# Kernel tuning notes

Hardware: AMD Instinct MI355X
Metric: run time of the kernel (lower is better)

The kernel has to match this reference:

```python
import jax, jax.numpy as jnp
import numpy as np

HIDDEN = 512
DETER = 1024
STOCH = 32
OBS = 1024
ACT = 64
B, T = 64, 256


def _linear_params(key, out_dim, in_dim):
    kw, kb = jax.random.split(key)
    scale = 1.0 / np.sqrt(in_dim)
    W = jax.random.uniform(kw, (out_dim, in_dim), jnp.float32, -scale, scale)
    b = jax.random.uniform(kb, (out_dim,), jnp.float32, -scale, scale)
    return W, b


def setup_inputs() -> dict:
    key = jax.random.key(0)
    ks = jax.random.split(key, 12)
    obs_embeds = jax.random.normal(ks[0], (B, T, OBS), jnp.float32)
    action_embs = jax.random.normal(ks[1], (B, T, ACT), jnp.float32)
    noise_prior = jax.random.normal(ks[2], (B, T, STOCH), jnp.float32)
    noise_post = jax.random.normal(ks[3], (B, T, STOCH), jnp.float32)
    W_sa, b_sa = _linear_params(ks[4], DETER, STOCH + ACT)
    W_ih, b_ih = _linear_params(ks[5], 3 * DETER, DETER)
    W_hh, b_hh = _linear_params(ks[6], 3 * DETER, DETER)
    Wp1, bp1 = _linear_params(ks[7], HIDDEN, DETER)
    Wp2, bp2 = _linear_params(ks[8], 2 * STOCH, HIDDEN)
    Wq1, bq1 = _linear_params(ks[9], HIDDEN, DETER + OBS)
    Wq2, bq2 = _linear_params(ks[10], 2 * STOCH, HIDDEN)
    return {
        "obs_embeds": obs_embeds, "action_embs": action_embs,
        "noise_prior": noise_prior, "noise_post": noise_post,
        "W_sa": W_sa, "b_sa": b_sa,
        "W_ih": W_ih, "b_ih": b_ih, "W_hh": W_hh, "b_hh": b_hh,
        "Wp1": Wp1, "bp1": bp1, "Wp2": Wp2, "bp2": bp2,
        "Wq1": Wq1, "bq1": bq1, "Wq2": Wq2, "bq2": bq2,
    }


def _rollout(obs_embeds, action_embs, noise_prior, noise_post,
             W_sa, b_sa, W_ih, b_ih, W_hh, b_hh,
             Wp1, bp1, Wp2, bp2, Wq1, bq1, Wq2, bq2):
    S = Wp2.shape[0] // 2
    eps = 1e-5

    def gru(x, h):  # torch GRUCell: gates ordered r, z, n
        gi = x @ W_ih.T + b_ih
        gh = h @ W_hh.T + b_hh
        ir, iz, inn = jnp.split(gi, 3, axis=-1)
        hr, hz, hn = jnp.split(gh, 3, axis=-1)
        r = jax.nn.sigmoid(ir + hr)
        z = jax.nn.sigmoid(iz + hz)
        n = jnp.tanh(inn + r * hn)
        return (1.0 - z) * n + z * h

    def step(carry, inp):
        deter, stoch = carry
        obs, act, n_p, n_q = inp
        # prior: h_t = f(s_{t-1}, a_{t-1}, h_{t-1})
        emb = jax.nn.relu(jnp.concatenate([stoch, act], -1) @ W_sa.T + b_sa)
        deter = gru(emb, deter)
        pm_s = jax.nn.relu(deter @ Wp1.T + bp1) @ Wp2.T + bp2
        p_mean = pm_s[..., :S]
        p_std = jax.nn.softplus(pm_s[..., S:]) + eps
        p_stoch = p_mean + p_std * n_p
        # posterior: p(s_t | h_t, o_t)
        qm_s = jax.nn.relu(jnp.concatenate([deter, obs], -1) @ Wq1.T + bq1) @ Wq2.T + bq2
        q_mean = qm_s[..., :S]
        q_std = jax.nn.softplus(qm_s[..., S:]) + eps
        q_stoch = q_mean + q_std * n_q
        out = jnp.concatenate([deter, p_mean, p_std, p_stoch, q_mean, q_std, q_stoch], -1)
        return (deter, q_stoch), out

    batch = obs_embeds.shape[0]
    deter0 = jnp.zeros((batch, W_hh.shape[1]), obs_embeds.dtype)
    stoch0 = jnp.zeros((batch, S), obs_embeds.dtype)
    xs = (
        jnp.swapaxes(obs_embeds, 0, 1),
        jnp.swapaxes(action_embs, 0, 1),
        jnp.swapaxes(noise_prior, 0, 1),
        jnp.swapaxes(noise_post, 0, 1),
    )
    _, outs = jax.lax.scan(step, (deter0, stoch0), xs)
    return jnp.swapaxes(outs, 0, 1)  # [B, T, deter + 6*stoch]


def reference(obs_embeds, action_embs, noise_prior, noise_post,
              W_sa, b_sa, W_ih, b_ih, W_hh, b_hh,
              Wp1, bp1, Wp2, bp2, Wq1, bq1, Wq2, bq2):
    return _rollout(obs_embeds, action_embs, noise_prior, noise_post,
                    W_sa, b_sa, W_ih, b_ih, W_hh, b_hh,
                    Wp1, bp1, Wp2, bp2, Wq1, bq1, Wq2, bq2)
```

## Files before the change

kernel.cpp:

```cpp
#include <hip/hip_runtime.h>
#include <math.h>

#define B_   64
#define T_   256
#define OUTD 1216

typedef unsigned short ushort_t;
typedef unsigned int   uint32;
typedef __attribute__((ext_vector_type(8))) short bfrag;
typedef __attribute__((ext_vector_type(4))) float f32x4;
typedef __attribute__((ext_vector_type(4))) unsigned short us4;

__device__ __forceinline__ float sigmoidf_(float x) { return 1.0f / (1.0f + __expf(-x)); }
__device__ __forceinline__ float softplusf_(float x) { return (x > 20.0f) ? x : log1pf(__expf(x)); }
__device__ __forceinline__ ushort_t f2bf(float f) {
    uint32 u = __float_as_uint(f);
    u += 0x7fffu + ((u >> 16) & 1u);
    return (ushort_t)(u >> 16);
}
__device__ __forceinline__ float bf2f(ushort_t u) { return __uint_as_float(((uint32)u) << 16); }

__global__ void kwprep(const float* __restrict__ Wih, const float* __restrict__ Whh,
                       const float* __restrict__ Wp1, const float* __restrict__ Wq1,
                       const float* __restrict__ Wp2, const float* __restrict__ Wq2,
                       const float* __restrict__ Wsa,
                       ushort_t* Wih_b, ushort_t* Whh_b, ushort_t* Wp1_b, ushort_t* Wq1_b,
                       ushort_t* W2sw, ushort_t* Wsasw) {
    int stride = gridDim.x * blockDim.x;
    int gid = blockIdx.x * blockDim.x + threadIdx.x;
    for (int i = gid; i < 3072 * 1024; i += stride) Wih_b[i] = f2bf(Wih[i]);
    for (int i = gid; i < 3072 * 1024; i += stride) Whh_b[i] = f2bf(Whh[i]);
    for (int i = gid; i < 512 * 1024; i += stride) Wp1_b[i] = f2bf(Wp1[i]);
    for (int i = gid; i < 512 * 2048; i += stride) Wq1_b[i] = f2bf(Wq1[i]);
    for (int i = gid; i < 65536; i += stride) {
        int head = i >> 15, g = (i >> 9) & 63, o = (i >> 3) & 63, ii = i & 7;
        const float* src = head ? Wq2 : Wp2;
        W2sw[i] = f2bf(src[o * 512 + g * 8 + ii]);
    }
    for (int i = gid; i < 98304; i += stride) {
        int g = i >> 13, j = (i >> 3) & 1023, ii = i & 7;
        Wsasw[i] = f2bf(Wsa[j * 96 + g * 8 + ii]);
    }
}

__global__ void kinit(const float* __restrict__ act, const float* __restrict__ Wsa,
                      const float* __restrict__ bsa,
                      ushort_t* emb_sw, ushort_t* det_sw0, float* det_fp0) {
    int gid = blockIdx.x * 256 + threadIdx.x;
    int j = gid >> 6, b = gid & 63;
    float acc = bsa[j];
    const float* a = act + (size_t)b * T_ * 64;
    const float* w = Wsa + j * 96 + 32;
#pragma unroll 8
    for (int c = 0; c < 64; ++c) acc += a[c] * w[c];
    emb_sw[((j >> 3) * 64 + b) * 8 + (j & 7)] = f2bf(fmaxf(acc, 0.f));
    det_sw0[gid] = 0;
    det_fp0[gid] = 0.f;
}

__global__ __launch_bounds__(256) void kgru(int t,
        const ushort_t* __restrict__ Wih, const ushort_t* __restrict__ Whh,
        const float* __restrict__ bih, const float* __restrict__ bhh,
        const ushort_t* __restrict__ emb_sw, const ushort_t* __restrict__ det_sw_in,
        const float* __restrict__ det_fp_in,
        ushort_t* __restrict__ det_sw_out, float* __restrict__ det_fp_out,
        const float* __restrict__ obs, ushort_t* __restrict__ obs_sw,
        float* __restrict__ out) {
    if (blockIdx.x >= 64) {
        int kb = (blockIdx.x - 64) * 64;
        int tx = threadIdx.x & 63, ty = threadIdx.x >> 6;
        for (int b = ty; b < 64; b += 4) {
            int k = kb + tx;
            float v = obs[((size_t)b * T_ + t) * 1024 + k];
            obs_sw[((k >> 3) * 64 + b) * 8 + (k & 7)] = f2bf(v);
        }
        return;
    }
    __shared__ float red[2 * 24 * 256];
    const int tid = threadIdx.x;
    const int lane = tid & 63, w = tid >> 6;
    const int m = lane & 15, quad = lane >> 4;
    const int j0 = blockIdx.x * 16;

    f32x4 acc[2][3][4];
#pragma unroll
    for (int a2 = 0; a2 < 2; ++a2)
#pragma unroll
        for (int g = 0; g < 3; ++g)
#pragma unroll
            for (int n = 0; n < 4; ++n) acc[a2][g][n] = (f32x4){0.f, 0.f, 0.f, 0.f};

    const int kb0 = w * 256;
    const ushort_t* arow[2][3];
#pragma unroll
    for (int g = 0; g < 3; ++g) {
        arow[0][g] = Wih + (size_t)(g * 1024 + j0 + m) * 1024 + kb0 + quad * 8;
        arow[1][g] = Whh + (size_t)(g * 1024 + j0 + m) * 1024 + kb0 + quad * 8;
    }
    const ushort_t* bx = emb_sw + ((kb0 >> 3) + quad) * 512 + m * 8;
    const ushort_t* bh = det_sw_in + ((kb0 >> 3) + quad) * 512 + m * 8;

#pragma unroll
    for (int it = 0; it < 8; ++it) {
        bfrag a[2][3], vx[4], vh[4];
#pragma unroll
        for (int g = 0; g < 3; ++g) {
            a[0][g] = *(const bfrag*)(arow[0][g] + it * 32);
            a[1][g] = *(const bfrag*)(arow[1][g] + it * 32);
        }
#pragma unroll
        for (int n = 0; n < 4; ++n) {
            vx[n] = *(const bfrag*)(bx + it * 2048 + n * 128);
            vh[n] = *(const bfrag*)(bh + it * 2048 + n * 128);
        }
#pragma unroll
        for (int g = 0; g < 3; ++g)
#pragma unroll
            for (int n = 0; n < 4; ++n) {
                acc[0][g][n] = __builtin_amdgcn_mfma_f32_16x16x32_bf16(a[0][g], vx[n], acc[0][g][n], 0, 0, 0);
                acc[1][g][n] = __builtin_amdgcn_mfma_f32_16x16x32_bf16(a[1][g], vh[n], acc[1][g][n], 0, 0, 0);
            }
    }

    if (w & 1) {
        float* dst = red + (w >> 1) * 6144;
#pragma unroll
        for (int a2 = 0; a2 < 2; ++a2)
#pragma unroll
            for (int g = 0; g < 3; ++g)
#pragma unroll
                for (int n = 0; n < 4; ++n)
                    *(f32x4*)(dst + ((a2 * 3 + g) * 4 + n) * 256 + lane * 4) = acc[a2][g][n];
    }
    __syncthreads();
    if (!(w & 1)) {
        float* dst = red + (w >> 1) * 6144;
#pragma unroll
        for (int a2 = 0; a2 < 2; ++a2)
#pragma unroll
            for (int g = 0; g < 3; ++g)
#pragma unroll
                for (int n = 0; n < 4; ++n) {
                    float* pp = dst + ((a2 * 3 + g) * 4 + n) * 256 + lane * 4;
                    f32x4 v = *(const f32x4*)pp;
                    v += acc[a2][g][n];
                    *(f32x4*)pp = v;
                }
    }
    __syncthreads();

    int b = tid >> 2, jq = tid & 3;
    int nt = b >> 4, bl = b & 15;
    int lsrc = (jq * 16 + bl) * 4;
    float gg[2][3][4];
#pragma unroll
    for (int a2 = 0; a2 < 2; ++a2)
#pragma unroll
        for (int g = 0; g < 3; ++g) {
            f32x4 v0 = *(const f32x4*)(red + ((a2 * 3 + g) * 4 + nt) * 256 + lsrc);
            f32x4 v1 = *(const f32x4*)(red + 6144 + ((a2 * 3 + g) * 4 + nt) * 256 + lsrc);
#pragma unroll
            for (int i = 0; i < 4; ++i) gg[a2][g][i] = v0[i] + v1[i];
        }
    f32x4 bi[3], bh2[3];
#pragma unroll
    for (int g = 0; g < 3; ++g) {
        bi[g] = *(const f32x4*)(bih + g * 1024 + j0 + jq * 4);
        bh2[g] = *(const f32x4*)(bhh + g * 1024 + j0 + jq * 4);
    }
    f32x4 h4;
    us4 dq;
#pragma unroll
    for (int i = 0; i < 4; ++i) {
        int j = j0 + jq * 4 + i;
        float r = sigmoidf_(gg[0][0][i] + bi[0][i] + gg[1][0][i] + bh2[0][i]);
        float z = sigmoidf_(gg[0][1][i] + bi[1][i] + gg[1][1][i] + bh2[1][i]);
        float n = tanhf(gg[0][2][i] + bi[2][i] + r * (gg[1][2][i] + bh2[2][i]));
        float hp = det_fp_in[j * 64 + b];
        float h = (1.f - z) * n + z * hp;
        h4[i] = h;
        dq[i] = f2bf(h);
        det_fp_out[j * 64 + b] = h;
    }
    *(f32x4*)(out + ((size_t)b * T_ + t) * OUTD + j0 + jq * 4) = h4;
    int kbase = j0 + jq * 4;
    *(us4*)(det_sw_out + ((kbase >> 3) * 64 + b) * 8 + (kbase & 7)) = dq;
}

__global__ __launch_bounds__(256) void khid(
        const ushort_t* __restrict__ Wp1b, const float* __restrict__ bp1,
        const ushort_t* __restrict__ Wq1b, const float* __restrict__ bq1,
        const ushort_t* __restrict__ det_sw, const ushort_t* __restrict__ obs_sw,
        float* __restrict__ pm1, float* __restrict__ qm1) {
    __shared__ float red[4 * 4 * 256];
    const int tid = threadIdx.x;
    const int lane = tid & 63, w = tid >> 6;
    const int m = lane & 15, quad = lane >> 4;
    const bool isq = blockIdx.x >= 32;
    const int j0 = (isq ? blockIdx.x - 32 : blockIdx.x) * 16;

    f32x4 acc[4];
#pragma unroll
    for (int n = 0; n < 4; ++n) acc[n] = (f32x4){0.f, 0.f, 0.f, 0.f};

    if (!isq) {
        const ushort_t* ar = Wp1b + (size_t)(j0 + m) * 1024 + w * 256 + quad * 8;
        const ushort_t* bb = det_sw + ((w * 32) + quad) * 512 + m * 8;
#pragma unroll
        for (int it = 0; it < 8; ++it) {
            bfrag a = *(const bfrag*)(ar + it * 32);
#pragma unroll
            for (int n = 0; n < 4; ++n) {
                bfrag v = *(const bfrag*)(bb + it * 2048 + n * 128);
                acc[n] = __builtin_amdgcn_mfma_f32_16x16x32_bf16(a, v, acc[n], 0, 0, 0);
            }
        }
    } else {
        int kb0 = w * 512;
        const ushort_t* bsrc = (w < 2) ? det_sw : obs_sw;
        int kloc = (w < 2) ? kb0 : kb0 - 1024;
        const ushort_t* ar = Wq1b + (size_t)(j0 + m) * 2048 + kb0 + quad * 8;
        const ushort_t* bb = bsrc + ((kloc >> 3) + quad) * 512 + m * 8;
#pragma unroll
        for (int it = 0; it < 16; ++it) {
            bfrag a = *(const bfrag*)(ar + it * 32);
#pragma unroll
            for (int n = 0; n < 4; ++n) {
                bfrag v = *(const bfrag*)(bb + it * 2048 + n * 128);
                acc[n] = __builtin_amdgcn_mfma_f32_16x16x32_bf16(a, v, acc[n], 0, 0, 0);
            }
        }
    }
#pragma unroll
    for (int n = 0; n < 4; ++n)
        *(f32x4*)(red + (w * 4 + n) * 256 + lane * 4) = acc[n];
    __syncthreads();

    int b = tid >> 2, jq = tid & 3;
    int nt = b >> 4, lsrc = (jq * 16 + (b & 15)) * 4;
    f32x4 s = (f32x4){0.f, 0.f, 0.f, 0.f};
#pragma unroll
    for (int w2 = 0; w2 < 4; ++w2) s += *(const f32x4*)(red + (w2 * 4 + nt) * 256 + lsrc);
    f32x4 bv = *(const f32x4*)((isq ? bq1 : bp1) + j0 + jq * 4);
    f32x4 r;
#pragma unroll
    for (int i = 0; i < 4; ++i) r[i] = fmaxf(s[i] + bv[i], 0.f);
    *(f32x4*)((isq ? qm1 : pm1) + (size_t)b * 512 + j0 + jq * 4) = r;
}

__global__ __launch_bounds__(256) void khead(int t,
        const float* __restrict__ pm1, const float* __restrict__ qm1,
        const float* __restrict__ bp2, const float* __restrict__ bq2,
        const ushort_t* __restrict__ W2sw, const ushort_t* __restrict__ Wsasw,
        const float* __restrict__ bsa,
        const float* __restrict__ n_p, const float* __restrict__ n_q,
        const float* __restrict__ act,
        float* __restrict__ out, ushort_t* __restrict__ emb_sw) {
    __shared__ float sh[1024 + 128 + 96];
    float* s_p = sh;
    float* s_q = sh + 512;
    float* s_head = sh + 1024;
    float* s_in = sh + 1152;
    const int b = blockIdx.x, tid = threadIdx.x;
    if (tid < 128) ((f32x4*)s_p)[tid] = ((const f32x4*)(pm1 + (size_t)b * 512))[tid];
    else ((f32x4*)s_q)[tid - 128] = ((const f32x4*)(qm1 + (size_t)b * 512))[tid - 128];
    if (t + 1 < T_ && tid < 64) s_in[32 + tid] = act[((size_t)b * T_ + t + 1) * 64 + tid];
    __syncthreads();
    if (tid < 128) {
        int head = tid >> 6, o = tid & 63;
        const ushort_t* wp = W2sw + head * 32768 + o * 8;
        const float* hv = head ? s_q : s_p;
        float acc2 = (head ? bq2 : bp2)[o];
#pragma unroll 4
        for (int g = 0; g < 64; ++g) {
            bfrag w8 = *(const bfrag*)(wp + g * 512);
#pragma unroll
            for (int i2 = 0; i2 < 8; ++i2) acc2 += hv[g * 8 + i2] * bf2f((ushort_t)w8[i2]);
        }
        s_head[tid] = acc2;
    }
    __syncthreads();
    if (tid < 64) {
        int s = tid & 31, isq = tid >> 5;
        float mean = s_head[isq * 64 + s];
        float raw = s_head[isq * 64 + 32 + s];
        float sd = softplusf_(raw) + 1e-5f;
        float noise = (isq ? n_q : n_p)[((size_t)b * T_ + t) * 32 + s];
        float st = mean + sd * noise;
        float* o = out + ((size_t)b * T_ + t) * OUTD + 1024 + isq * 96;
        o[s] = mean;
        o[32 + s] = sd;
        o[64 + s] = st;
        if (isq) s_in[s] = st;
    }
    __syncthreads();
    if (t + 1 < T_) {
#pragma unroll
        for (int q = 0; q < 4; ++q) {
            int j = q * 256 + tid;
            float acc2 = bsa[j];
#pragma unroll
            for (int g = 0; g < 12; ++g) {
                bfrag w8 = *(const bfrag*)(Wsasw + ((size_t)g * 1024 + j) * 8);
#pragma unroll
                for (int i2 = 0; i2 < 8; ++i2) acc2 += s_in[g * 8 + i2] * bf2f((ushort_t)w8[i2]);
            }
            emb_sw[((j >> 3) * 64 + b) * 8 + (j & 7)] = f2bf(fmaxf(acc2, 0.f));
        }
    }
}

extern "C" void kernel_launch(void* const* d_in, const int* in_sizes, int n_in,
                              void* d_out, int out_size, void* d_ws, size_t ws_size,
                              hipStream_t stream) {
    const float* obs = (const float*)d_in[0];
    const float* act = (const float*)d_in[1];
    const float* n_p = (const float*)d_in[2];
    const float* n_q = (const float*)d_in[3];
    const float* W_sa = (const float*)d_in[4];
    const float* b_sa = (const float*)d_in[5];
    const float* W_ih = (const float*)d_in[6];
    const float* b_ih = (const float*)d_in[7];
    const float* W_hh = (const float*)d_in[8];
    const float* b_hh = (const float*)d_in[9];
    const float* Wp1 = (const float*)d_in[10];
    const float* bp1 = (const float*)d_in[11];
    const float* Wp2 = (const float*)d_in[12];
    const float* bp2 = (const float*)d_in[13];
    const float* Wq1 = (const float*)d_in[14];
    const float* bq1 = (const float*)d_in[15];
    const float* Wq2 = (const float*)d_in[16];
    const float* bq2 = (const float*)d_in[17];
    float* out = (float*)d_out;

    char* p = (char*)d_ws;
    ushort_t* Wih_b = (ushort_t*)p;  p += (size_t)3145728 * 2;
    ushort_t* Whh_b = (ushort_t*)p;  p += (size_t)3145728 * 2;
    ushort_t* Wp1_b = (ushort_t*)p;  p += (size_t)524288 * 2;
    ushort_t* Wq1_b = (ushort_t*)p;  p += (size_t)1048576 * 2;
    ushort_t* W2sw  = (ushort_t*)p;  p += (size_t)65536 * 2;
    ushort_t* Wsasw = (ushort_t*)p;  p += (size_t)98304 * 2;
    ushort_t* emb_sw = (ushort_t*)p; p += (size_t)65536 * 2;
    ushort_t* obs_sw = (ushort_t*)p; p += (size_t)65536 * 2;
    ushort_t* det_sw0 = (ushort_t*)p; p += (size_t)65536 * 2;
    ushort_t* det_sw1 = (ushort_t*)p; p += (size_t)65536 * 2;
    float* det_fp0 = (float*)p; p += (size_t)65536 * 4;
    float* det_fp1 = (float*)p; p += (size_t)65536 * 4;
    float* pm1 = (float*)p; p += (size_t)32768 * 4;
    float* qm1 = (float*)p; p += (size_t)32768 * 4;

    kwprep<<<1024, 256, 0, stream>>>(W_ih, W_hh, Wp1, Wq1, Wp2, Wq2, W_sa,
                                     Wih_b, Whh_b, Wp1_b, Wq1_b, W2sw, Wsasw);
    kinit<<<256, 256, 0, stream>>>(act, W_sa, b_sa, emb_sw, det_sw0, det_fp0);

    for (int t = 0; t < T_; ++t) {
        ushort_t* dsw_in = (t & 1) ? det_sw1 : det_sw0;
        ushort_t* dsw_out = (t & 1) ? det_sw0 : det_sw1;
        float* dfp_in = (t & 1) ? det_fp1 : det_fp0;
        float* dfp_out = (t & 1) ? det_fp0 : det_fp1;
        kgru<<<80, 256, 0, stream>>>(t, Wih_b, Whh_b, b_ih, b_hh, emb_sw, dsw_in, dfp_in,
                                     dsw_out, dfp_out, obs, obs_sw, out);
        khid<<<64, 256, 0, stream>>>(Wp1_b, bp1, Wq1_b, bq1, dsw_out, obs_sw, pm1, qm1);
        khead<<<64, 256, 0, stream>>>(t, pm1, qm1, bp2, bq2, W2sw, Wsasw, b_sa,
                                      n_p, n_q, act, out, emb_sw);
    }
}
```

Baseline: 10.24 ms.

## Fuse per-step kernels into one persistent rollout kernel with grid barriers

Replaces the 768 per-timestep launches (GRU, hidden, head kernels) with a single persistent kernel of 64 blocks that loops over all time steps. Stages are separated by a software grid barrier built on global atomics. Obs conversion moves into the head stage for the next step. This removes kernel launch overhead and launch gaps. The risks are that the barrier needs all 64 blocks co-resident, that spin-wait barriers carry their own latency, and that the obs conversion now uses only 64 blocks.

```diff
diff --git a/kernel.cpp b/kernel.cpp
--- a/kernel.cpp
+++ b/kernel.cpp
@@ -20,14 +20,32 @@
 }
 __device__ __forceinline__ float bf2f(ushort_t u) { return __uint_as_float(((uint32)u) << 16); }
 
+__device__ __forceinline__ void gbar(uint32* barf, int gen) {
+    __syncthreads();
+    if (threadIdx.x == 0) {
+        __threadfence();
+        uint32 old = __hip_atomic_fetch_add(barf + (gen & 1) * 32, 1u,
+                                            __ATOMIC_ACQ_REL, __HIP_MEMORY_SCOPE_AGENT);
+        if (old == 63u) {
+            __hip_atomic_store(barf + (gen & 1) * 32, 0u, __ATOMIC_RELAXED, __HIP_MEMORY_SCOPE_AGENT);
+            __hip_atomic_store(barf + 64, (uint32)gen, __ATOMIC_RELEASE, __HIP_MEMORY_SCOPE_AGENT);
+        }
+        while ((int)__hip_atomic_load(barf + 64, __ATOMIC_ACQUIRE, __HIP_MEMORY_SCOPE_AGENT) < gen)
+            __builtin_amdgcn_s_sleep(1);
+    }
+    __syncthreads();
+    __threadfence();
+}
+
 __global__ void kwprep(const float* __restrict__ Wih, const float* __restrict__ Whh,
                        const float* __restrict__ Wp1, const float* __restrict__ Wq1,
                        const float* __restrict__ Wp2, const float* __restrict__ Wq2,
                        const float* __restrict__ Wsa,
                        ushort_t* Wih_b, ushort_t* Whh_b, ushort_t* Wp1_b, ushort_t* Wq1_b,
-                       ushort_t* W2sw, ushort_t* Wsasw) {
+                       ushort_t* W2sw, ushort_t* Wsasw, uint32* barf) {
     int stride = gridDim.x * blockDim.x;
     int gid = blockIdx.x * blockDim.x + threadIdx.x;
+    if (gid < 256) barf[gid] = 0u;
     for (int i = gid; i < 3072 * 1024; i += stride) Wih_b[i] = f2bf(Wih[i]);
     for (int i = gid; i < 3072 * 1024; i += stride) Whh_b[i] = f2bf(Whh[i]);
     for (int i = gid; i < 512 * 1024; i += stride) Wp1_b[i] = f2bf(Wp1[i]);
@@ -43,270 +61,268 @@
     }
 }
 
-__global__ void kinit(const float* __restrict__ act, const float* __restrict__ Wsa,
-                      const float* __restrict__ bsa,
-                      ushort_t* emb_sw, ushort_t* det_sw0, float* det_fp0) {
-    int gid = blockIdx.x * 256 + threadIdx.x;
-    int j = gid >> 6, b = gid & 63;
-    float acc = bsa[j];
-    const float* a = act + (size_t)b * T_ * 64;
-    const float* w = Wsa + j * 96 + 32;
-#pragma unroll 8
-    for (int c = 0; c < 64; ++c) acc += a[c] * w[c];
-    emb_sw[((j >> 3) * 64 + b) * 8 + (j & 7)] = f2bf(fmaxf(acc, 0.f));
-    det_sw0[gid] = 0;
-    det_fp0[gid] = 0.f;
-}
-
-__global__ __launch_bounds__(256) void kgru(int t,
-        const ushort_t* __restrict__ Wih, const ushort_t* __restrict__ Whh,
-        const float* __restrict__ bih, const float* __restrict__ bhh,
-        const ushort_t* __restrict__ emb_sw, const ushort_t* __restrict__ det_sw_in,
-        const float* __restrict__ det_fp_in,
-        ushort_t* __restrict__ det_sw_out, float* __restrict__ det_fp_out,
-        const float* __restrict__ obs, ushort_t* __restrict__ obs_sw,
-        float* __restrict__ out) {
-    if (blockIdx.x >= 64) {
-        int kb = (blockIdx.x - 64) * 64;
-        int tx = threadIdx.x & 63, ty = threadIdx.x >> 6;
-        for (int b = ty; b < 64; b += 4) {
-            int k = kb + tx;
-            float v = obs[((size_t)b * T_ + t) * 1024 + k];
-            obs_sw[((k >> 3) * 64 + b) * 8 + (k & 7)] = f2bf(v);
-        }
-        return;
-    }
-    __shared__ float red[2 * 24 * 256];
-    const int tid = threadIdx.x;
+__global__ __launch_bounds__(256, 1) void krollout(
+        const ushort_t* Wih, const ushort_t* Whh,
+        const float* bih, const float* bhh,
+        const ushort_t* Wp1b, const float* bp1,
+        const ushort_t* Wq1b, const float* bq1,
+        const ushort_t* W2sw, const float* bp2, const float* bq2,
+        const ushort_t* Wsasw, const float* Wsa, const float* bsa,
+        const float* obs, const float* act,
+        const float* n_p, const float* n_q,
+        ushort_t* emb_sw, ushort_t* obs_sw,
+        ushort_t* det_sw0, ushort_t* det_sw1,
+        float* det_fp0, float* det_fp1,
+        float* pm1, float* qm1,
+        float* out, uint32* barf) {
+    __shared__ float red[12288];
+    const int bid = blockIdx.x, tid = threadIdx.x;
     const int lane = tid & 63, w = tid >> 6;
     const int m = lane & 15, quad = lane >> 4;
-    const int j0 = blockIdx.x * 16;
-
-    f32x4 acc[2][3][4];
-#pragma unroll
-    for (int a2 = 0; a2 < 2; ++a2)
-#pragma unroll
-        for (int g = 0; g < 3; ++g)
-#pragma unroll
-            for (int n = 0; n < 4; ++n) acc[a2][g][n] = (f32x4){0.f, 0.f, 0.f, 0.f};
-
-    const int kb0 = w * 256;
-    const ushort_t* arow[2][3];
-#pragma unroll
-    for (int g = 0; g < 3; ++g) {
-        arow[0][g] = Wih + (size_t)(g * 1024 + j0 + m) * 1024 + kb0 + quad * 8;
-        arow[1][g] = Whh + (size_t)(g * 1024 + j0 + m) * 1024 + kb0 + quad * 8;
-    }
-    const ushort_t* bx = emb_sw + ((kb0 >> 3) + quad) * 512 + m * 8;
-    const ushort_t* bh = det_sw_in + ((kb0 >> 3) + quad) * 512 + m * 8;
-
-#pragma unroll
-    for (int it = 0; it < 8; ++it) {
-        bfrag a[2][3], vx[4], vh[4];
-#pragma unroll
-        for (int g = 0; g < 3; ++g) {
-            a[0][g] = *(const bfrag*)(arow[0][g] + it * 32);
-            a[1][g] = *(const bfrag*)(arow[1][g] + it * 32);
-        }
-#pragma unroll
-        for (int n = 0; n < 4; ++n) {
-            vx[n] = *(const bfrag*)(bx + it * 2048 + n * 128);
-            vh[n] = *(const bfrag*)(bh + it * 2048 + n * 128);
-        }
-#pragma unroll
-        for (int g = 0; g < 3; ++g)
-#pragma unroll
-            for (int n = 0; n < 4; ++n) {
-                acc[0][g][n] = __builtin_amdgcn_mfma_f32_16x16x32_bf16(a[0][g], vx[n], acc[0][g][n], 0, 0, 0);
-                acc[1][g][n] = __builtin_amdgcn_mfma_f32_16x16x32_bf16(a[1][g], vh[n], acc[1][g][n], 0, 0, 0);
-            }
-    }
-
-    if (w & 1) {
-        float* dst = red + (w >> 1) * 6144;
-#pragma unroll
-        for (int a2 = 0; a2 < 2; ++a2)
-#pragma unroll
-            for (int g = 0; g < 3; ++g)
-#pragma unroll
-                for (int n = 0; n < 4; ++n)
-                    *(f32x4*)(dst + ((a2 * 3 + g) * 4 + n) * 256 + lane * 4) = acc[a2][g][n];
-    }
-    __syncthreads();
-    if (!(w & 1)) {
-        float* dst = red + (w >> 1) * 6144;
-#pragma unroll
-        for (int a2 = 0; a2 < 2; ++a2)
-#pragma unroll
-            for (int g = 0; g < 3; ++g)
+
+    *(f32x4*)(det_fp0 + bid * 1024 + tid * 4) = (f32x4){0.f, 0.f, 0.f, 0.f};
+    *(us4*)(det_sw0 + bid * 1024 + tid * 4) = (us4){0, 0, 0, 0};
+    {
+        int j0i = bid * 16;
+        for (int c4 = 0; c4 < 4; ++c4) {
+            int idx = c4 * 256 + tid;
+            int j = j0i + (idx >> 6), b2 = idx & 63;
+            float acc = bsa[j];
+            const float* a = act + (size_t)b2 * T_ * 64;
+            const float* ww = Wsa + j * 96 + 32;
+            for (int c = 0; c < 64; ++c) acc += a[c] * ww[c];
+            emb_sw[((j >> 3) * 64 + b2) * 8 + (j & 7)] = f2bf(fmaxf(acc, 0.f));
+        }
+        float4 v = *(const float4*)(obs + (size_t)bid * T_ * 1024 + tid * 4);
+        us4 o4; o4[0] = f2bf(v.x); o4[1] = f2bf(v.y); o4[2] = f2bf(v.z); o4[3] = f2bf(v.w);
+        int k = tid * 4;
+        *(us4*)(obs_sw + ((k >> 3) * 64 + bid) * 8 + (k & 7)) = o4;
+    }
+    int gen = 1;
+    gbar(barf, gen); ++gen;
+
+    for (int t = 0; t < T_; ++t) {
+        ushort_t* dsw_in  = (t & 1) ? det_sw1 : det_sw0;
+        ushort_t* dsw_out = (t & 1) ? det_sw0 : det_sw1;
+        float* dfp_in  = (t & 1) ? det_fp1 : det_fp0;
+        float* dfp_out = (t & 1) ? det_fp0 : det_fp1;
+
+        {
+            const int j0 = bid * 16;
+            f32x4 acc[2][3][4];
+#pragma unroll
+            for (int a2 = 0; a2 < 2; ++a2)
+#pragma unroll
+                for (int g = 0; g < 3; ++g)
+#pragma unroll
+                    for (int n = 0; n < 4; ++n) acc[a2][g][n] = (f32x4){0.f, 0.f, 0.f, 0.f};
+
+            const int kb0 = w * 256;
+            const ushort_t* arow[2][3];
+#pragma unroll
+            for (int g = 0; g < 3; ++g) {
+                arow[0][g] = Wih + (size_t)(g * 1024 + j0 + m) * 1024 + kb0 + quad * 8;
+                arow[1][g] = Whh + (size_t)(g * 1024 + j0 + m) * 1024 + kb0 + quad * 8;
+            }
+            const ushort_t* bx = emb_sw + ((kb0 >> 3) + quad) * 512 + m * 8;
+            const ushort_t* bh = dsw_in + ((kb0 >> 3) + quad) * 512 + m * 8;
+
+#pragma unroll
+            for (int it = 0; it < 8; ++it) {
+                bfrag a[2][3], vx[4], vh[4];
+#pragma unroll
+                for (int g = 0; g < 3; ++g) {
+                    a[0][g] = *(const bfrag*)(arow[0][g] + it * 32);
+                    a[1][g] = *(const bfrag*)(arow[1][g] + it * 32);
+                }
 #pragma unroll
                 for (int n = 0; n < 4; ++n) {
-                    float* pp = dst + ((a2 * 3 + g) * 4 + n) * 256 + lane * 4;
-                    f32x4 v = *(const f32x4*)pp;
-                    v += acc[a2][g][n];
-                    *(f32x4*)pp = v;
-                }
-    }
-    __syncthreads();
-
-    int b = tid >> 2, jq = tid & 3;
-    int nt = b >> 4, bl = b & 15;
-    int lsrc = (jq * 16 + bl) * 4;
-    float gg[2][3][4];
-#pragma unroll
-    for (int a2 = 0; a2 < 2; ++a2)
-#pragma unroll
-        for (int g = 0; g < 3; ++g) {
-            f32x4 v0 = *(const f32x4*)(red + ((a2 * 3 + g) * 4 + nt) * 256 + lsrc);
-            f32x4 v1 = *(const f32x4*)(red + 6144 + ((a2 * 3 + g) * 4 + nt) * 256 + lsrc);
-#pragma unroll
-            for (int i = 0; i < 4; ++i) gg[a2][g][i] = v0[i] + v1[i];
-        }
-    f32x4 bi[3], bh2[3];
-#pragma unroll
-    for (int g = 0; g < 3; ++g) {
-        bi[g] = *(const f32x4*)(bih + g * 1024 + j0 + jq * 4);
-        bh2[g] = *(const f32x4*)(bhh + g * 1024 + j0 + jq * 4);
-    }
-    f32x4 h4;
-    us4 dq;
-#pragma unroll
-    for (int i = 0; i < 4; ++i) {
-        int j = j0 + jq * 4 + i;
-        float r = sigmoidf_(gg[0][0][i] + bi[0][i] + gg[1][0][i] + bh2[0][i]);
-        float z = sigmoidf_(gg[0][1][i] + bi[1][i] + gg[1][1][i] + bh2[1][i]);
-        float n = tanhf(gg[0][2][i] + bi[2][i] + r * (gg[1][2][i] + bh2[2][i]));
-        float hp = det_fp_in[j * 64 + b];
-        float h = (1.f - z) * n + z * hp;
-        h4[i] = h;
-        dq[i] = f2bf(h);
-        det_fp_out[j * 64 + b] = h;
-    }
-    *(f32x4*)(out + ((size_t)b * T_ + t) * OUTD + j0 + jq * 4) = h4;
-    int kbase = j0 + jq * 4;
-    *(us4*)(det_sw_out + ((kbase >> 3) * 64 + b) * 8 + (kbase & 7)) = dq;
-}
-
-__global__ __launch_bounds__(256) void khid(
-        const ushort_t* __restrict__ Wp1b, const float* __restrict__ bp1,
-        const ushort_t* __restrict__ Wq1b, const float* __restrict__ bq1,
-        const ushort_t* __restrict__ det_sw, const ushort_t* __restrict__ obs_sw,
-        float* __restrict__ pm1, float* __restrict__ qm1) {
-    __shared__ float red[4 * 4 * 256];
-    const int tid = threadIdx.x;
-    const int lane = tid & 63, w = tid >> 6;
-    const int m = lane & 15, quad = lane >> 4;
-    const bool isq = blockIdx.x >= 32;
-    const int j0 = (isq ? blockIdx.x - 32 : blockIdx.x) * 16;
-
-    f32x4 acc[4];
-#pragma unroll
-    for (int n = 0; n < 4; ++n) acc[n] = (f32x4){0.f, 0.f, 0.f, 0.f};
-
-    if (!isq) {
-        const ushort_t* ar = Wp1b + (size_t)(j0 + m) * 1024 + w * 256 + quad * 8;
-        const ushort_t* bb = det_sw + ((w * 32) + quad) * 512 + m * 8;
-#pragma unroll
-        for (int it = 0; it < 8; ++it) {
-            bfrag a = *(const bfrag*)(ar + it * 32);
-#pragma unroll
-            for (int n = 0; n < 4; ++n) {
-                bfrag v = *(const bfrag*)(bb + it * 2048 + n * 128);
-                acc[n] = __builtin_amdgcn_mfma_f32_16x16x32_bf16(a, v, acc[n], 0, 0, 0);
-            }
-        }
-    } else {
-        int kb0 = w * 512;
-        const ushort_t* bsrc = (w < 2) ? det_sw : obs_sw;
-        int kloc = (w < 2) ? kb0 : kb0 - 1024;
-        const ushort_t* ar = Wq1b + (size_t)(j0 + m) * 2048 + kb0 + quad * 8;
-        const ushort_t* bb = bsrc + ((kloc >> 3) + quad) * 512 + m * 8;
-#pragma unroll
-        for (int it = 0; it < 16; ++it) {
-            bfrag a = *(const bfrag*)(ar + it * 32);
-#pragma unroll
-            for (int n = 0; n < 4; ++n) {
-                bfrag v = *(const bfrag*)(bb + it * 2048 + n * 128);
-                acc[n] = __builtin_amdgcn_mfma_f32_16x16x32_bf16(a, v, acc[n], 0, 0, 0);
-            }
-        }
-    }
-#pragma unroll
-    for (int n = 0; n < 4; ++n)
-        *(f32x4*)(red + (w * 4 + n) * 256 + lane * 4) = acc[n];
-    __syncthreads();
-
-    int b = tid >> 2, jq = tid & 3;
-    int nt = b >> 4, lsrc = (jq * 16 + (b & 15)) * 4;
-    f32x4 s = (f32x4){0.f, 0.f, 0.f, 0.f};
-#pragma unroll
-    for (int w2 = 0; w2 < 4; ++w2) s += *(const f32x4*)(red + (w2 * 4 + nt) * 256 + lsrc);
-    f32x4 bv = *(const f32x4*)((isq ? bq1 : bp1) + j0 + jq * 4);
-    f32x4 r;
-#pragma unroll
-    for (int i = 0; i < 4; ++i) r[i] = fmaxf(s[i] + bv[i], 0.f);
-    *(f32x4*)((isq ? qm1 : pm1) + (size_t)b * 512 + j0 + jq * 4) = r;
-}
-
-__global__ __launch_bounds__(256) void khead(int t,
-        const float* __restrict__ pm1, const float* __restrict__ qm1,
-        const float* __restrict__ bp2, const float* __restrict__ bq2,
-        const ushort_t* __restrict__ W2sw, const ushort_t* __restrict__ Wsasw,
-        const float* __restrict__ bsa,
-        const float* __restrict__ n_p, const float* __restrict__ n_q,
-        const float* __restrict__ act,
-        float* __restrict__ out, ushort_t* __restrict__ emb_sw) {
-    __shared__ float sh[1024 + 128 + 96];
-    float* s_p = sh;
-    float* s_q = sh + 512;
-    float* s_head = sh + 1024;
-    float* s_in = sh + 1152;
-    const int b = blockIdx.x, tid = threadIdx.x;
-    if (tid < 128) ((f32x4*)s_p)[tid] = ((const f32x4*)(pm1 + (size_t)b * 512))[tid];
-    else ((f32x4*)s_q)[tid - 128] = ((const f32x4*)(qm1 + (size_t)b * 512))[tid - 128];
-    if (t + 1 < T_ && tid < 64) s_in[32 + tid] = act[((size_t)b * T_ + t + 1) * 64 + tid];
-    __syncthreads();
-    if (tid < 128) {
-        int head = tid >> 6, o = tid & 63;
-        const ushort_t* wp = W2sw + head * 32768 + o * 8;
-        const float* hv = head ? s_q : s_p;
-        float acc2 = (head ? bq2 : bp2)[o];
+                    vx[n] = *(const bfrag*)(bx + it * 2048 + n * 128);
+                    vh[n] = *(const bfrag*)(bh + it * 2048 + n * 128);
+                }
+#pragma unroll
+                for (int g = 0; g < 3; ++g)
+#pragma unroll
+                    for (int n = 0; n < 4; ++n) {
+                        acc[0][g][n] = __builtin_amdgcn_mfma_f32_16x16x32_bf16(a[0][g], vx[n], acc[0][g][n], 0, 0, 0);
+                        acc[1][g][n] = __builtin_amdgcn_mfma_f32_16x16x32_bf16(a[1][g], vh[n], acc[1][g][n], 0, 0, 0);
+                    }
+            }
+            if (w & 1) {
+                float* dst = red + (w >> 1) * 6144;
+#pragma unroll
+                for (int a2 = 0; a2 < 2; ++a2)
+#pragma unroll
+                    for (int g = 0; g < 3; ++g)
+#pragma unroll
+                        for (int n = 0; n < 4; ++n)
+                            *(f32x4*)(dst + ((a2 * 3 + g) * 4 + n) * 256 + lane * 4) = acc[a2][g][n];
+            }
+            __syncthreads();
+            if (!(w & 1)) {
+                float* dst = red + (w >> 1) * 6144;
+#pragma unroll
+                for (int a2 = 0; a2 < 2; ++a2)
+#pragma unroll
+                    for (int g = 0; g < 3; ++g)
+#pragma unroll
+                        for (int n = 0; n < 4; ++n) {
+                            float* pp = dst + ((a2 * 3 + g) * 4 + n) * 256 + lane * 4;
+                            f32x4 v = *(const f32x4*)pp;
+                            v += acc[a2][g][n];
+                            *(f32x4*)pp = v;
+                        }
+            }
+            __syncthreads();
+            int b = tid >> 2, jq = tid & 3;
+            int nt = b >> 4, bl = b & 15;
+            int lsrc = (jq * 16 + bl) * 4;
+            float gg[2][3][4];
+#pragma unroll
+            for (int a2 = 0; a2 < 2; ++a2)
+#pragma unroll
+                for (int g = 0; g < 3; ++g) {
+                    f32x4 v0 = *(const f32x4*)(red + ((a2 * 3 + g) * 4 + nt) * 256 + lsrc);
+                    f32x4 v1 = *(const f32x4*)(red + 6144 + ((a2 * 3 + g) * 4 + nt) * 256 + lsrc);
+#pragma unroll
+                    for (int i = 0; i < 4; ++i) gg[a2][g][i] = v0[i] + v1[i];
+                }
+            f32x4 bi[3], bh2[3];
+#pragma unroll
+            for (int g = 0; g < 3; ++g) {
+                bi[g] = *(const f32x4*)(bih + g * 1024 + j0 + jq * 4);
+                bh2[g] = *(const f32x4*)(bhh + g * 1024 + j0 + jq * 4);
+            }
+            f32x4 h4;
+            us4 dq;
+#pragma unroll
+            for (int i = 0; i < 4; ++i) {
+                int j = j0 + jq * 4 + i;
+                float r = sigmoidf_(gg[0][0][i] + bi[0][i] + gg[1][0][i] + bh2[0][i]);
+                float z = sigmoidf_(gg[0][1][i] + bi[1][i] + gg[1][1][i] + bh2[1][i]);
+                float n = tanhf(gg[0][2][i] + bi[2][i] + r * (gg[1][2][i] + bh2[2][i]));
+                float hp = dfp_in[j * 64 + b];
+                float h = (1.f - z) * n + z * hp;
+                h4[i] = h;
+                dq[i] = f2bf(h);
+                dfp_out[j * 64 + b] = h;
+            }
+            *(f32x4*)(out + ((size_t)b * T_ + t) * OUTD + j0 + jq * 4) = h4;
+            int kbase = j0 + jq * 4;
+            *(us4*)(dsw_out + ((kbase >> 3) * 64 + b) * 8 + (kbase & 7)) = dq;
+        }
+        gbar(barf, gen); ++gen;
+
+        {
+            const bool isq = bid >= 32;
+            const int j0 = (isq ? bid - 32 : bid) * 16;
+            f32x4 acc[4];
+#pragma unroll
+            for (int n = 0; n < 4; ++n) acc[n] = (f32x4){0.f, 0.f, 0.f, 0.f};
+
+            if (!isq) {
+                const ushort_t* ar = Wp1b + (size_t)(j0 + m) * 1024 + w * 256 + quad * 8;
+                const ushort_t* bb = dsw_out + ((w * 32) + quad) * 512 + m * 8;
+#pragma unroll
+                for (int it = 0; it < 8; ++it) {
+                    bfrag a = *(const bfrag*)(ar + it * 32);
+#pragma unroll
+                    for (int n = 0; n < 4; ++n) {
+                        bfrag v = *(const bfrag*)(bb + it * 2048 + n * 128);
+                        acc[n] = __builtin_amdgcn_mfma_f32_16x16x32_bf16(a, v, acc[n], 0, 0, 0);
+                    }
+                }
+            } else {
+                int kb0 = w * 512;
+                const ushort_t* bsrc = (w < 2) ? dsw_out : obs_sw;
+                int kloc = (w < 2) ? kb0 : kb0 - 1024;
+                const ushort_t* ar = Wq1b + (size_t)(j0 + m) * 2048 + kb0 + quad * 8;
+                const ushort_t* bb = bsrc + ((kloc >> 3) + quad) * 512 + m * 8;
+#pragma unroll
+                for (int it = 0; it < 16; ++it) {
+                    bfrag a = *(const bfrag*)(ar + it * 32);
+#pragma unroll
+                    for (int n = 0; n < 4; ++n) {
+                        bfrag v = *(const bfrag*)(bb + it * 2048 + n * 128);
+                        acc[n] = __builtin_amdgcn_mfma_f32_16x16x32_bf16(a, v, acc[n], 0, 0, 0);
+                    }
+                }
+            }
+#pragma unroll
+            for (int n = 0; n < 4; ++n)
+                *(f32x4*)(red + (w * 4 + n) * 256 + lane * 4) = acc[n];
+            __syncthreads();
+            int b = tid >> 2, jq = tid & 3;
+            int nt = b >> 4, lsrc = (jq * 16 + (b & 15)) * 4;
+            f32x4 s = (f32x4){0.f, 0.f, 0.f, 0.f};
+#pragma unroll
+            for (int w2 = 0; w2 < 4; ++w2) s += *(const f32x4*)(red + (w2 * 4 + nt) * 256 + lsrc);
+            f32x4 bv = *(const f32x4*)((isq ? bq1 : bp1) + j0 + jq * 4);
+            f32x4 r;
+#pragma unroll
+            for (int i = 0; i < 4; ++i) r[i] = fmaxf(s[i] + bv[i], 0.f);
+            *(f32x4*)((isq ? qm1 : pm1) + (size_t)b * 512 + j0 + jq * 4) = r;
+        }
+        gbar(barf, gen); ++gen;
+
+        {
+            float* s_p = red;
+            float* s_q = red + 512;
+            float* s_head = red + 1024;
+            float* s_in = red + 1152;
+            const int bb = bid;
+            if (tid < 128) ((f32x4*)s_p)[tid] = ((const f32x4*)(pm1 + (size_t)bb * 512))[tid];
+            else ((f32x4*)s_q)[tid - 128] = ((const f32x4*)(qm1 + (size_t)bb * 512))[tid - 128];
+            if (t + 1 < T_ && tid < 64) s_in[32 + tid] = act[((size_t)bb * T_ + t + 1) * 64 + tid];
+            __syncthreads();
+            if (tid < 128) {
+                int head = tid >> 6, o = tid & 63;
+                const ushort_t* wp = W2sw + head * 32768 + o * 8;
+                const float* hv = head ? s_q : s_p;
+                float acc2 = (head ? bq2 : bp2)[o];
 #pragma unroll 4
-        for (int g = 0; g < 64; ++g) {
-            bfrag w8 = *(const bfrag*)(wp + g * 512);
-#pragma unroll
-            for (int i2 = 0; i2 < 8; ++i2) acc2 += hv[g * 8 + i2] * bf2f((ushort_t)w8[i2]);
-        }
-        s_head[tid] = acc2;
-    }
-    __syncthreads();
-    if (tid < 64) {
-        int s = tid & 31, isq = tid >> 5;
-        float mean = s_head[isq * 64 + s];
-        float raw = s_head[isq * 64 + 32 + s];
-        float sd = softplusf_(raw) + 1e-5f;
-        float noise = (isq ? n_q : n_p)[((size_t)b * T_ + t) * 32 + s];
-        float st = mean + sd * noise;
-        float* o = out + ((size_t)b * T_ + t) * OUTD + 1024 + isq * 96;
-        o[s] = mean;
-        o[32 + s] = sd;
-        o[64 + s] = st;
-        if (isq) s_in[s] = st;
-    }
-    __syncthreads();
-    if (t + 1 < T_) {
-#pragma unroll
-        for (int q = 0; q < 4; ++q) {
-            int j = q * 256 + tid;
-            float acc2 = bsa[j];
-#pragma unroll
-            for (int g = 0; g < 12; ++g) {
-                bfrag w8 = *(const bfrag*)(Wsasw + ((size_t)g * 1024 + j) * 8);
-#pragma unroll
-                for (int i2 = 0; i2 < 8; ++i2) acc2 += s_in[g * 8 + i2] * bf2f((ushort_t)w8[i2]);
-            }
-            emb_sw[((j >> 3) * 64 + b) * 8 + (j & 7)] = f2bf(fmaxf(acc2, 0.f));
-        }
+                for (int g = 0; g < 64; ++g) {
+                    bfrag w8 = *(const bfrag*)(wp + g * 512);
+#pragma unroll
+                    for (int i2 = 0; i2 < 8; ++i2) acc2 += hv[g * 8 + i2] * bf2f((ushort_t)w8[i2]);
+                }
+                s_head[tid] = acc2;
+            }
+            __syncthreads();
+            if (tid < 64) {
+                int s = tid & 31, isq2 = tid >> 5;
+                float mean = s_head[isq2 * 64 + s];
+                float raw = s_head[isq2 * 64 + 32 + s];
+                float sd = softplusf_(raw) + 1e-5f;
+                float noise = (isq2 ? n_q : n_p)[((size_t)bb * T_ + t) * 32 + s];
+                float st = mean + sd * noise;
+                float* o = out + ((size_t)bb * T_ + t) * OUTD + 1024 + isq2 * 96;
+                o[s] = mean;
+                o[32 + s] = sd;
+                o[64 + s] = st;
+                if (isq2) s_in[s] = st;
+            }
+            __syncthreads();
+            if (t + 1 < T_) {
+#pragma unroll
+                for (int q = 0; q < 4; ++q) {
+                    int j = q * 256 + tid;
+                    float acc2 = bsa[j];
+#pragma unroll
+                    for (int g = 0; g < 12; ++g) {
+                        bfrag w8 = *(const bfrag*)(Wsasw + ((size_t)g * 1024 + j) * 8);
+#pragma unroll
+                        for (int i2 = 0; i2 < 8; ++i2) acc2 += s_in[g * 8 + i2] * bf2f((ushort_t)w8[i2]);
+                    }
+                    emb_sw[((j >> 3) * 64 + bb) * 8 + (j & 7)] = f2bf(fmaxf(acc2, 0.f));
+                }
+                float4 v = *(const float4*)(obs + ((size_t)bb * T_ + t + 1) * 1024 + tid * 4);
+                us4 o4; o4[0] = f2bf(v.x); o4[1] = f2bf(v.y); o4[2] = f2bf(v.z); o4[3] = f2bf(v.w);
+                int k = tid * 4;
+                *(us4*)(obs_sw + ((k >> 3) * 64 + bb) * 8 + (k & 7)) = o4;
+            }
+        }
+        if (t + 1 < T_) { gbar(barf, gen); ++gen; }
     }
 }
 
@@ -334,6 +350,7 @@
     float* out = (float*)d_out;
 
     char* p = (char*)d_ws;
+    uint32* barf = (uint32*)p;       p += 256 * 4;
     ushort_t* Wih_b = (ushort_t*)p;  p += (size_t)3145728 * 2;
     ushort_t* Whh_b = (ushort_t*)p;  p += (size_t)3145728 * 2;
     ushort_t* Wp1_b = (ushort_t*)p;  p += (size_t)524288 * 2;
@@ -350,18 +367,10 @@
     float* qm1 = (float*)p; p += (size_t)32768 * 4;
 
     kwprep<<<1024, 256, 0, stream>>>(W_ih, W_hh, Wp1, Wq1, Wp2, Wq2, W_sa,
-                                     Wih_b, Whh_b, Wp1_b, Wq1_b, W2sw, Wsasw);
-    kinit<<<256, 256, 0, stream>>>(act, W_sa, b_sa, emb_sw, det_sw0, det_fp0);
-
-    for (int t = 0; t < T_; ++t) {
-        ushort_t* dsw_in = (t & 1) ? det_sw1 : det_sw0;
-        ushort_t* dsw_out = (t & 1) ? det_sw0 : det_sw1;
-        float* dfp_in = (t & 1) ? det_fp1 : det_fp0;
-        float* dfp_out = (t & 1) ? det_fp0 : det_fp1;
-        kgru<<<80, 256, 0, stream>>>(t, Wih_b, Whh_b, b_ih, b_hh, emb_sw, dsw_in, dfp_in,
-                                     dsw_out, dfp_out, obs, obs_sw, out);
-        khid<<<64, 256, 0, stream>>>(Wp1_b, bp1, Wq1_b, bq1, dsw_out, obs_sw, pm1, qm1);
-        khead<<<64, 256, 0, stream>>>(t, pm1, qm1, bp2, bq2, W2sw, Wsasw, b_sa,
-                                      n_p, n_q, act, out, emb_sw);
-    }
-}
+                                     Wih_b, Whh_b, Wp1_b, Wq1_b, W2sw, Wsasw, barf);
+    krollout<<<64, 256, 0, stream>>>(Wih_b, Whh_b, b_ih, b_hh, Wp1_b, bp1, Wq1_b, bq1,
+                                     W2sw, bp2, bq2, Wsasw, W_sa, b_sa,
+                                     obs, act, n_p, n_q,
+                                     emb_sw, obs_sw, det_sw0, det_sw1,
+                                     det_fp0, det_fp1, pm1, qm1, out, barf);
+}
```

Measured after the change: 22.42 ms. 119% more time.
